# Kernel tuning notes

Measured on AMD Instinct MI355X. Metric: run time of the kernel, lower is better.

The kernel has to match this reference:

```python
import jax, jax.numpy as jnp
import numpy as np

B, N, C = 32, 256, 4096
H = 16
HEAD_DIM = C // H  # 256 == N, required by the module's math
SCALE = HEAD_DIM ** -0.5


def setup_inputs() -> dict:
    key = jax.random.key(0)
    ks = jax.random.split(key, 7)
    std = C ** -0.5
    return {
        "x1": jax.random.normal(ks[0], (B, N, C), dtype=jnp.float32),
        "x2": jax.random.normal(ks[1], (B, N, C), dtype=jnp.float32),
        "Wq": jax.random.normal(ks[2], (C, C), dtype=jnp.float32) * std,
        "Wk": jax.random.normal(ks[3], (C, C), dtype=jnp.float32) * std,
        "Wv": jax.random.normal(ks[4], (C, C), dtype=jnp.float32) * std,
        "Wp": jax.random.normal(ks[5], (C, C), dtype=jnp.float32) * std,
        "bp": jnp.zeros((C,), dtype=jnp.float32),
    }


def reference(x1, x2, Wq, Wk, Wv, Wp, bp):
    b, n, c = x1.shape
    h, hd = H, HEAD_DIM
    # QKV projections (qkv_bias=False); q pre-scaled as in source
    q = (x1 @ Wq.T) * SCALE
    k = x2 @ Wk.T
    v = x2 @ Wv.T
    split = lambda t: t.reshape(b, n, h, hd).transpose(0, 2, 1, 3)  # b h n hd
    q, k, v = split(q), split(k), split(v)
    # channel-wise attention: q^T @ k over the token axis -> [b, h, hd, hd]
    attn = jax.nn.softmax(jnp.einsum("bhni,bhnj->bhij", q, k), axis=-1)
    # attn @ v: inner dim of attn (hd) contracts with token axis of v (n == hd)
    out = jnp.einsum("bhin,bhnc->bhic", attn, v)  # [b, h, hd, hd]
    out = out.transpose(0, 2, 1, 3).reshape(b, n, c)
    x = out @ Wp.T + bp
    return (x, attn)
```

## Files before the change

### kernel.cpp

```cpp
#include <hip/hip_runtime.h>

typedef __attribute__((ext_vector_type(4))) float f32x4;
typedef __attribute__((ext_vector_type(8))) short short8;
typedef __attribute__((ext_vector_type(4))) unsigned short ushort4v;

__device__ __forceinline__ unsigned short rne_bf16(float f) {
  unsigned int u = __builtin_bit_cast(unsigned int, f);
  u += 0x7FFFu + ((u >> 16) & 1u);
  return (unsigned short)(u >> 16);
}

__device__ __forceinline__ void async16(void* lds, const void* g) {
  __builtin_amdgcn_global_load_lds(
      (const __attribute__((address_space(1))) void*)g,
      (__attribute__((address_space(3))) void*)lds, 16, 0, 0);
}

__device__ __forceinline__ f32x4 mfma16(short8 a, short8 b, f32x4 c) {
  return __builtin_amdgcn_mfma_f32_16x16x32_bf16(a, b, c, 0, 0, 0);
}

__global__ __launch_bounds__(256) void cast_k(const float* __restrict__ in,
                                              unsigned short* __restrict__ out,
                                              int n4) {
  int stride = gridDim.x * 256;
  for (int i = blockIdx.x * 256 + threadIdx.x; i < n4; i += stride) {
    float4 v = ((const float4*)in)[i];
    ushort4v o = {rne_bf16(v.x), rne_bf16(v.y), rne_bf16(v.z), rne_bf16(v.w)};
    ((ushort4v*)out)[i] = o;
  }
}

template <int MODE>
__global__ __launch_bounds__(512, 2) void gemm256(const unsigned short* __restrict__ A,
                                                  const unsigned short* __restrict__ B,
                                                  float* __restrict__ outF,
                                                  unsigned short* __restrict__ outB,
                                                  const float* __restrict__ bias,
                                                  int K, int lda, int ldb,
                                                  float scale, int gx) {
  __shared__ unsigned short lds[65536];
  const int tid = threadIdx.x;
  const int lane = tid & 63;
  const int wid = tid >> 6;
  const int wm = wid >> 2;
  const int wn = wid & 3;
  int lin = blockIdx.x;
  lin = (lin & 7) * (gridDim.x >> 3) + (lin >> 3);
  const int bx = lin % gx;
  const int by = lin / gx;
  const int m0 = by * 256, n0 = bx * 256;
  const int NT = K >> 6;

  const int gsw8 = (((tid & 3) ^ ((tid >> 3) & 3))) * 8;
  const unsigned short* gA = A + (size_t)(m0 + (tid >> 2)) * lda + gsw8;
  const unsigned short* gB = B + (size_t)(n0 + (tid >> 2)) * ldb + gsw8;
  const size_t astep = (size_t)128 * lda;
  const size_t bstep = (size_t)128 * ldb;
  unsigned short* ld0 = &lds[tid * 8];

#define STG(Q) do { \
    const int kt_ = ((Q) >> 1) * 64 + ((Q) & 1) * 32; \
    const int off_ = (((Q) >> 1) & 1) * 32768 + ((Q) & 1) * 8192; \
    const unsigned short* sA_ = gA + kt_; \
    unsigned short* dA_ = ld0 + off_; \
    async16(dA_, sA_); async16(dA_ + 4096, sA_ + astep); \
    const unsigned short* sB_ = gB + kt_; \
    unsigned short* dB_ = ld0 + 16384 + off_; \
    async16(dB_, sB_); async16(dB_ + 4096, sB_ + bstep); } while (0)

  const int rl = lane & 15;
  const int ch = (lane >> 4) ^ ((rl >> 1) & 3);
  const int aidx = wm * 4096 + rl * 32 + ch * 8;
  const int bidx = 16384 + wn * 2048 + rl * 32 + ch * 8;

  short8 af[8], bf0[4], bf1[4];
#define READ_A(base) do { \
    _Pragma("unroll") \
    for (int r_ = 0; r_ < 8; ++r_) af[r_] = *(const short8*)&lds[(base) + aidx + r_ * 512]; \
  } while (0)
#define READ_B(base, dst) do { \
    _Pragma("unroll") \
    for (int s_ = 0; s_ < 4; ++s_) dst[s_] = *(const short8*)&lds[(base) + bidx + s_ * 512]; \
  } while (0)

  f32x4 acc[8][4];
#pragma unroll
  for (int r = 0; r < 8; ++r)
#pragma unroll
    for (int s = 0; s < 4; ++s) acc[r][s] = (f32x4){0.f, 0.f, 0.f, 0.f};

#define MFMA32(bfX) do { \
    __builtin_amdgcn_s_setprio(1); \
    _Pragma("unroll") \
    for (int r_ = 0; r_ < 8; ++r_) \
      _Pragma("unroll") \
      for (int s_ = 0; s_ < 4; ++s_) acc[r_][s_] = mfma16(af[r_], bfX[s_], acc[r_][s_]); \
    __builtin_amdgcn_s_setprio(0); \
  } while (0)

  STG(0); STG(1); STG(2);
  asm volatile("s_waitcnt vmcnt(4)" ::: "memory");
  __builtin_amdgcn_s_barrier();
  READ_B(0, bf0);

  for (int t = 0; t < NT; ++t) {
    const int bb = (t & 1) * 32768;
    READ_A(bb);
    READ_B(bb + 8192, bf1);
    if (t + 1 < NT) STG(2 * t + 3);
    __builtin_amdgcn_sched_barrier(0);
    MFMA32(bf0);
    if (t + 1 < NT) asm volatile("s_waitcnt vmcnt(4)" ::: "memory");
    else            asm volatile("s_waitcnt vmcnt(0)" ::: "memory");
    __builtin_amdgcn_s_barrier();
    READ_A(bb + 8192);
    if (t + 1 < NT) {
      READ_B(((t + 1) & 1) * 32768, bf0);
      if (t + 2 < NT) STG(2 * t + 4);
    }
    __builtin_amdgcn_sched_barrier(0);
    MFMA32(bf1);
    if (t + 1 < NT) {
      if (t + 2 < NT) asm volatile("s_waitcnt vmcnt(4)" ::: "memory");
      else            asm volatile("s_waitcnt vmcnt(0)" ::: "memory");
      __builtin_amdgcn_s_barrier();
    }
  }
#undef STG
#undef READ_A
#undef READ_B
#undef MFMA32

  const int fcol = lane & 15;
  const int frow = (lane >> 4) * 4;
#pragma unroll
  for (int r = 0; r < 8; ++r) {
#pragma unroll
    for (int s = 0; s < 4; ++s) {
      f32x4 v = acc[r][s];
      const int m = m0 + wm * 128 + r * 16 + frow;
      const int n = n0 + wn * 64 + s * 16 + fcol;
      if (MODE == 0) {
        ushort4v p;
#pragma unroll
        for (int j = 0; j < 4; ++j) p[j] = rne_bf16(v[j] * scale);
        size_t d = ((size_t)((m >> 8) * 16 + (n >> 8))) * 65536 +
                   (size_t)(n & 255) * 256 + (m & 255);
        *(ushort4v*)&outB[d] = p;
      } else {
        float bv = bias[n];
#pragma unroll
        for (int j = 0; j < 4; ++j) outF[(size_t)(m + j) * 4096 + n] = v[j] + bv;
      }
    }
  }
}

template <int MODE>
__global__ __launch_bounds__(256) void gemm_bt(const unsigned short* __restrict__ Ab,
                                               const unsigned short* __restrict__ Bb,
                                               float* __restrict__ outF,
                                               unsigned short* __restrict__ outB,
                                               int K, int lda, int ldb) {
  __shared__ short Ash[128 * 32];
  __shared__ short Bsh[128 * 32];

  const int tid = threadIdx.x;
  const int lane = tid & 63;
  const int wid = tid >> 6;
  const int z = blockIdx.z;
  const int m0 = blockIdx.y * 128;
  const int n0 = blockIdx.x * 128;

  const unsigned short* A = Ab + (size_t)z * 65536;
  const unsigned short* B = Bb + (size_t)z * 65536;

  const int wm = (wid >> 1) * 64;
  const int wn = (wid & 1) * 64;
  const int fcol = lane & 15;
  const int kslot = (lane >> 4) * 8;

  f32x4 acc[4][4];
#pragma unroll
  for (int r = 0; r < 4; ++r)
#pragma unroll
    for (int s = 0; s < 4; ++s) acc[r][s] = (f32x4){0.f, 0.f, 0.f, 0.f};

  const int arow = tid >> 2;
  const int acol = (tid & 3) * 8;
  const unsigned short* gA = A + (size_t)(m0 + arow) * lda + acol;
  const unsigned short* gB = B + (size_t)(n0 + arow) * ldb + acol;
  short* lA = &Ash[tid * 8];
  short* lB = &Bsh[tid * 8];

  for (int kt = 0; kt < K; kt += 32) {
    __syncthreads();
    async16(lA, gA + kt);
    async16(lA + 2048, gA + (size_t)64 * lda + kt);
    async16(lB, gB + kt);
    async16(lB + 2048, gB + (size_t)64 * ldb + kt);
    __syncthreads();

    short8 a[4], b[4];
#pragma unroll
    for (int r = 0; r < 4; ++r)
      a[r] = *(const short8*)&Ash[(wm + r * 16 + fcol) * 32 + kslot];
#pragma unroll
    for (int s = 0; s < 4; ++s)
      b[s] = *(const short8*)&Bsh[(wn + s * 16 + fcol) * 32 + kslot];
#pragma unroll
    for (int r = 0; r < 4; ++r)
#pragma unroll
      for (int s = 0; s < 4; ++s)
        acc[r][s] = __builtin_amdgcn_mfma_f32_16x16x32_bf16(a[r], b[s], acc[r][s], 0, 0, 0);
  }

  const int frow = (lane >> 4) * 4;
#pragma unroll
  for (int r = 0; r < 4; ++r) {
#pragma unroll
    for (int s = 0; s < 4; ++s) {
      f32x4 v = acc[r][s];
      const int m = m0 + wm + r * 16 + frow;
      const int n = n0 + wn + s * 16 + fcol;
      if (MODE == 1) {
        float* C = outF + (size_t)z * 65536;
#pragma unroll
        for (int j = 0; j < 4; ++j) C[(size_t)(m + j) * 256 + n] = v[j];
      } else {
        size_t base = ((size_t)((z >> 4) * 256 + m)) * 4096 + (z & 15) * 256 + n;
#pragma unroll
        for (int j = 0; j < 4; ++j) outB[base + (size_t)j * 4096] = rne_bf16(v[j]);
      }
    }
  }
}

__global__ __launch_bounds__(256) void softmax_k(float* __restrict__ S,
                                                 unsigned short* __restrict__ P) {
  const int lane = threadIdx.x & 63;
  const size_t row = (size_t)blockIdx.x * 4 + (threadIdx.x >> 6);
  float4 x = *(const float4*)&S[row * 256 + lane * 4];
  float mx = fmaxf(fmaxf(x.x, x.y), fmaxf(x.z, x.w));
#pragma unroll
  for (int off = 32; off; off >>= 1) mx = fmaxf(mx, __shfl_xor(mx, off, 64));
  float e0 = __expf(x.x - mx), e1 = __expf(x.y - mx);
  float e2 = __expf(x.z - mx), e3 = __expf(x.w - mx);
  float s = e0 + e1 + e2 + e3;
#pragma unroll
  for (int off = 32; off; off >>= 1) s += __shfl_xor(s, off, 64);
  const float inv = 1.0f / s;
  e0 *= inv; e1 *= inv; e2 *= inv; e3 *= inv;
  *(float4*)&S[row * 256 + lane * 4] = make_float4(e0, e1, e2, e3);
  ushort4v ob = {rne_bf16(e0), rne_bf16(e1), rne_bf16(e2), rne_bf16(e3)};
  *(ushort4v*)&P[row * 256 + lane * 4] = ob;
}

extern "C" void kernel_launch(void* const* d_in, const int* in_sizes, int n_in,
                              void* d_out, int out_size, void* d_ws, size_t ws_size,
                              hipStream_t stream) {
  const float* x1 = (const float*)d_in[0];
  const float* x2 = (const float*)d_in[1];
  const float* Wq = (const float*)d_in[2];
  const float* Wk = (const float*)d_in[3];
  const float* Wv = (const float*)d_in[4];
  const float* Wp = (const float*)d_in[5];
  const float* bp = (const float*)d_in[6];

  float* outX = (float*)d_out;
  float* outA = outX + (size_t)33554432;

  unsigned short* Qt  = (unsigned short*)d_ws;
  unsigned short* Kt  = Qt + 33554432;
  unsigned short* Vt  = Kt + 33554432;
  unsigned short* x1b = Vt + 33554432;
  unsigned short* x2b = x1b + 33554432;
  unsigned short* Wb  = x2b + 33554432;

  const float SCALE = 0.0625f;

  cast_k<<<2048, 256, 0, stream>>>(x1, x1b, 8388608);
  cast_k<<<2048, 256, 0, stream>>>(x2, x2b, 8388608);

  cast_k<<<2048, 256, 0, stream>>>(Wq, Wb, 4194304);
  gemm256<0><<<512, 512, 0, stream>>>(x1b, Wb, nullptr, Qt, nullptr,
                                      4096, 4096, 4096, SCALE, 16);
  cast_k<<<2048, 256, 0, stream>>>(Wk, Wb, 4194304);
  gemm256<0><<<512, 512, 0, stream>>>(x2b, Wb, nullptr, Kt, nullptr,
                                      4096, 4096, 4096, 1.0f, 16);
  cast_k<<<2048, 256, 0, stream>>>(Wv, Wb, 4194304);
  gemm256<0><<<512, 512, 0, stream>>>(x2b, Wb, nullptr, Vt, nullptr,
                                      4096, 4096, 4096, 1.0f, 16);

  gemm_bt<1><<<dim3(2, 2, 512), 256, 0, stream>>>(Qt, Kt, outA, nullptr, 256, 256, 256);
  softmax_k<<<32768, 256, 0, stream>>>(outA, x1b);
  gemm_bt<2><<<dim3(2, 2, 512), 256, 0, stream>>>(x1b, Vt, nullptr, x2b, 256, 256, 256);

  cast_k<<<2048, 256, 0, stream>>>(Wp, Wb, 4194304);
  gemm256<3><<<512, 512, 0, stream>>>(x2b, Wb, outX, nullptr, bp,
                                      4096, 4096, 4096, 1.0f, 16);
}
```

Measured before the change: 1.323 ms.

## Split GEMM main loop into finer phases with barrier-interleaved LDS reads and staging

Restructures the bf16 MFMA GEMM main loop into per-half-tile phases. Each phase reads half of the A fragments plus B, issues the A stage, runs 16 MFMAs, then reads the other A half and issues the B stage before the next 16 MFMAs. Extra block barriers and lgkmcnt waits are added in a ping-pong style schedule. The aim is to interleave LDS reads, global-to-LDS copies and MFMAs across waves while cutting fragment registers (one B buffer instead of two). The cost is more barriers per K step and exposed LDS read latency, since B is no longer prefetched.

```diff
diff --git a/kernel.cpp b/kernel.cpp
--- a/kernel.cpp
+++ b/kernel.cpp
@@ -59,14 +59,17 @@
   const size_t bstep = (size_t)128 * ldb;
   unsigned short* ld0 = &lds[tid * 8];
 
-#define STG(Q) do { \
+#define STG_A(Q) do { \
     const int kt_ = ((Q) >> 1) * 64 + ((Q) & 1) * 32; \
     const int off_ = (((Q) >> 1) & 1) * 32768 + ((Q) & 1) * 8192; \
     const unsigned short* sA_ = gA + kt_; \
     unsigned short* dA_ = ld0 + off_; \
-    async16(dA_, sA_); async16(dA_ + 4096, sA_ + astep); \
+    async16(dA_, sA_); async16(dA_ + 4096, sA_ + astep); } while (0)
+#define STG_B(Q) do { \
+    const int kt_ = ((Q) >> 1) * 64 + ((Q) & 1) * 32; \
+    const int off_ = 16384 + (((Q) >> 1) & 1) * 32768 + ((Q) & 1) * 8192; \
     const unsigned short* sB_ = gB + kt_; \
-    unsigned short* dB_ = ld0 + 16384 + off_; \
+    unsigned short* dB_ = ld0 + off_; \
     async16(dB_, sB_); async16(dB_ + 4096, sB_ + bstep); } while (0)
 
   const int rl = lane & 15;
@@ -74,14 +77,15 @@
   const int aidx = wm * 4096 + rl * 32 + ch * 8;
   const int bidx = 16384 + wn * 2048 + rl * 32 + ch * 8;
 
-  short8 af[8], bf0[4], bf1[4];
-#define READ_A(base) do { \
+  short8 af[8], bf[4];
+#define READ_A4(base, o) do { \
     _Pragma("unroll") \
-    for (int r_ = 0; r_ < 8; ++r_) af[r_] = *(const short8*)&lds[(base) + aidx + r_ * 512]; \
+    for (int r_ = 0; r_ < 4; ++r_) \
+      af[(o) + r_] = *(const short8*)&lds[(base) + aidx + ((o) + r_) * 512]; \
   } while (0)
-#define READ_B(base, dst) do { \
+#define READ_B4(base) do { \
     _Pragma("unroll") \
-    for (int s_ = 0; s_ < 4; ++s_) dst[s_] = *(const short8*)&lds[(base) + bidx + s_ * 512]; \
+    for (int s_ = 0; s_ < 4; ++s_) bf[s_] = *(const short8*)&lds[(base) + bidx + s_ * 512]; \
   } while (0)
 
   f32x4 acc[8][4];
@@ -90,47 +94,56 @@
 #pragma unroll
     for (int s = 0; s < 4; ++s) acc[r][s] = (f32x4){0.f, 0.f, 0.f, 0.f};
 
-#define MFMA32(bfX) do { \
+#define MFMA16(o) do { \
+    _Pragma("unroll") \
+    for (int r_ = 0; r_ < 4; ++r_) \
+      _Pragma("unroll") \
+      for (int s_ = 0; s_ < 4; ++s_) \
+        acc[(o) + r_][s_] = mfma16(af[(o) + r_], bf[s_], acc[(o) + r_][s_]); \
+  } while (0)
+
+#define PHASE(P_, rb_, doStage_) do { \
+    READ_A4((rb_), 0); \
+    READ_B4((rb_)); \
+    if (doStage_) STG_A((P_) + 3); \
+    __builtin_amdgcn_sched_barrier(0); \
+    __builtin_amdgcn_s_barrier(); \
+    asm volatile("s_waitcnt lgkmcnt(0)" ::: "memory"); \
+    __builtin_amdgcn_sched_barrier(0); \
     __builtin_amdgcn_s_setprio(1); \
-    _Pragma("unroll") \
-    for (int r_ = 0; r_ < 8; ++r_) \
-      _Pragma("unroll") \
-      for (int s_ = 0; s_ < 4; ++s_) acc[r_][s_] = mfma16(af[r_], bfX[s_], acc[r_][s_]); \
+    MFMA16(0); \
     __builtin_amdgcn_s_setprio(0); \
+    __builtin_amdgcn_s_barrier(); \
+    READ_A4((rb_), 4); \
+    if (doStage_) STG_B((P_) + 3); \
+    __builtin_amdgcn_sched_barrier(0); \
+    __builtin_amdgcn_s_barrier(); \
+    asm volatile("s_waitcnt lgkmcnt(0)" ::: "memory"); \
+    __builtin_amdgcn_sched_barrier(0); \
+    __builtin_amdgcn_s_setprio(1); \
+    MFMA16(4); \
+    __builtin_amdgcn_s_setprio(0); \
+    if (doStage_) asm volatile("s_waitcnt vmcnt(4)" ::: "memory"); \
+    else          asm volatile("s_waitcnt vmcnt(0)" ::: "memory"); \
+    __builtin_amdgcn_s_barrier(); \
   } while (0)
 
-  STG(0); STG(1); STG(2);
+  STG_A(0); STG_B(0); STG_A(1); STG_B(1); STG_A(2); STG_B(2);
   asm volatile("s_waitcnt vmcnt(4)" ::: "memory");
   __builtin_amdgcn_s_barrier();
-  READ_B(0, bf0);
-
+
+  const int PMAX = 2 * NT - 1;
   for (int t = 0; t < NT; ++t) {
     const int bb = (t & 1) * 32768;
-    READ_A(bb);
-    READ_B(bb + 8192, bf1);
-    if (t + 1 < NT) STG(2 * t + 3);
-    __builtin_amdgcn_sched_barrier(0);
-    MFMA32(bf0);
-    if (t + 1 < NT) asm volatile("s_waitcnt vmcnt(4)" ::: "memory");
-    else            asm volatile("s_waitcnt vmcnt(0)" ::: "memory");
-    __builtin_amdgcn_s_barrier();
-    READ_A(bb + 8192);
-    if (t + 1 < NT) {
-      READ_B(((t + 1) & 1) * 32768, bf0);
-      if (t + 2 < NT) STG(2 * t + 4);
-    }
-    __builtin_amdgcn_sched_barrier(0);
-    MFMA32(bf1);
-    if (t + 1 < NT) {
-      if (t + 2 < NT) asm volatile("s_waitcnt vmcnt(4)" ::: "memory");
-      else            asm volatile("s_waitcnt vmcnt(0)" ::: "memory");
-      __builtin_amdgcn_s_barrier();
-    }
-  }
-#undef STG
-#undef READ_A
-#undef READ_B
-#undef MFMA32
+    PHASE(2 * t,     bb,        (2 * t + 3) <= PMAX);
+    PHASE(2 * t + 1, bb + 8192, (2 * t + 4) <= PMAX);
+  }
+#undef STG_A
+#undef STG_B
+#undef READ_A4
+#undef READ_B4
+#undef MFMA16
+#undef PHASE
 
   const int fcol = lane & 15;
   const int frow = (lane >> 4) * 4;
```

Result: slower. 1.349 ms (+2.0%).

## Fuse QK^T, softmax and PV into a single attention kernel

Applied to the files above, without the earlier changes.

Replaces the separate score GEMM, softmax kernel and attn@V GEMM with one kernel per (head, 64-row block). Scores stay in registers and the softmax uses cross-wave reductions through LDS. Normalized probabilities go to the fp32 output and to padded bf16 LDS, which feed the PV MFMA loop directly, with V double-buffered. This removes the fp32 score round trip and the bf16 P round trip through global memory and two launches. In exchange, K is reloaded per row block and LDS use is large (~69KB), which limits occupancy.

```diff
diff --git a/kernel.cpp b/kernel.cpp
--- a/kernel.cpp
+++ b/kernel.cpp
@@ -157,104 +157,174 @@
   }
 }
 
-template <int MODE>
-__global__ __launch_bounds__(256) void gemm_bt(const unsigned short* __restrict__ Ab,
-                                               const unsigned short* __restrict__ Bb,
-                                               float* __restrict__ outF,
-                                               unsigned short* __restrict__ outB,
-                                               int K, int lda, int ldb) {
-  __shared__ short Ash[128 * 32];
-  __shared__ short Bsh[128 * 32];
-
+__global__ __launch_bounds__(256) void attn_fused(const unsigned short* __restrict__ Qt,
+                                                  const unsigned short* __restrict__ Kt,
+                                                  const unsigned short* __restrict__ Vt,
+                                                  float* __restrict__ outA,
+                                                  unsigned short* __restrict__ outXb) {
+  __shared__ unsigned short sh[34560];
   const int tid = threadIdx.x;
   const int lane = tid & 63;
   const int wid = tid >> 6;
-  const int z = blockIdx.z;
-  const int m0 = blockIdx.y * 128;
-  const int n0 = blockIdx.x * 128;
-
-  const unsigned short* A = Ab + (size_t)z * 65536;
-  const unsigned short* B = Bb + (size_t)z * 65536;
-
-  const int wm = (wid >> 1) * 64;
-  const int wn = (wid & 1) * 64;
+  const int z = blockIdx.y;
+  const int m0 = blockIdx.x * 64;
+  const int wm = wid >> 1;
+  const int wn = wid & 1;
   const int fcol = lane & 15;
   const int kslot = (lane >> 4) * 8;
-
-  f32x4 acc[4][4];
-#pragma unroll
-  for (int r = 0; r < 4; ++r)
-#pragma unroll
-    for (int s = 0; s < 4; ++s) acc[r][s] = (f32x4){0.f, 0.f, 0.f, 0.f};
-
-  const int arow = tid >> 2;
-  const int acol = (tid & 3) * 8;
-  const unsigned short* gA = A + (size_t)(m0 + arow) * lda + acol;
-  const unsigned short* gB = B + (size_t)(n0 + arow) * ldb + acol;
-  short* lA = &Ash[tid * 8];
-  short* lB = &Bsh[tid * 8];
-
-  for (int kt = 0; kt < K; kt += 32) {
-    __syncthreads();
-    async16(lA, gA + kt);
-    async16(lA + 2048, gA + (size_t)64 * lda + kt);
-    async16(lB, gB + kt);
-    async16(lB + 2048, gB + (size_t)64 * ldb + kt);
-    __syncthreads();
-
-    short8 a[4], b[4];
-#pragma unroll
-    for (int r = 0; r < 4; ++r)
-      a[r] = *(const short8*)&Ash[(wm + r * 16 + fcol) * 32 + kslot];
-#pragma unroll
-    for (int s = 0; s < 4; ++s)
-      b[s] = *(const short8*)&Bsh[(wn + s * 16 + fcol) * 32 + kslot];
-#pragma unroll
-    for (int r = 0; r < 4; ++r)
-#pragma unroll
-      for (int s = 0; s < 4; ++s)
-        acc[r][s] = __builtin_amdgcn_mfma_f32_16x16x32_bf16(a[r], b[s], acc[r][s], 0, 0, 0);
-  }
-
   const int frow = (lane >> 4) * 4;
-#pragma unroll
-  for (int r = 0; r < 4; ++r) {
-#pragma unroll
-    for (int s = 0; s < 4; ++s) {
-      f32x4 v = acc[r][s];
-      const int m = m0 + wm + r * 16 + frow;
-      const int n = n0 + wn + s * 16 + fcol;
-      if (MODE == 1) {
-        float* C = outF + (size_t)z * 65536;
-#pragma unroll
-        for (int j = 0; j < 4; ++j) C[(size_t)(m + j) * 256 + n] = v[j];
-      } else {
-        size_t base = ((size_t)((z >> 4) * 256 + m)) * 4096 + (z & 15) * 256 + n;
-#pragma unroll
-        for (int j = 0; j < 4; ++j) outB[base + (size_t)j * 4096] = rne_bf16(v[j]);
+
+  const unsigned short* Qh = Qt + (size_t)z * 65536;
+  const unsigned short* Kh = Kt + (size_t)z * 65536;
+  const unsigned short* Vh = Vt + (size_t)z * 65536;
+  float* redM = (float*)&sh[33536];
+  float* redS = redM + 128;
+
+  f32x4 acc[2][8];
+#pragma unroll
+  for (int r = 0; r < 2; ++r)
+#pragma unroll
+    for (int s = 0; s < 8; ++s) acc[r][s] = (f32x4){0.f, 0.f, 0.f, 0.f};
+
+  {
+    const int arow = tid >> 2;
+    const int acol = (tid & 3) * 8;
+    const unsigned short* gQ = Qh + (size_t)(m0 + arow) * 256 + acol;
+    const unsigned short* gK = Kh + (size_t)arow * 256 + acol;
+    unsigned short* lA = &sh[tid * 8];
+    unsigned short* lB = &sh[2048 + tid * 8];
+
+    for (int kt = 0; kt < 256; kt += 32) {
+      __syncthreads();
+      async16(lA, gQ + kt);
+      async16(lB, gK + kt);
+      async16(lB + 2048, gK + (size_t)64 * 256 + kt);
+      async16(lB + 4096, gK + (size_t)128 * 256 + kt);
+      async16(lB + 6144, gK + (size_t)192 * 256 + kt);
+      __syncthreads();
+
+      short8 a[2], b[8];
+#pragma unroll
+      for (int r = 0; r < 2; ++r)
+        a[r] = *(const short8*)&sh[(wm * 32 + r * 16 + fcol) * 32 + kslot];
+#pragma unroll
+      for (int s = 0; s < 8; ++s)
+        b[s] = *(const short8*)&sh[2048 + (wn * 128 + s * 16 + fcol) * 32 + kslot];
+#pragma unroll
+      for (int r = 0; r < 2; ++r)
+#pragma unroll
+        for (int s = 0; s < 8; ++s)
+          acc[r][s] = mfma16(a[r], b[s], acc[r][s]);
+    }
+  }
+  __syncthreads();
+
+#pragma unroll
+  for (int r = 0; r < 2; ++r) {
+#pragma unroll
+    for (int j = 0; j < 4; ++j) {
+      float m = acc[r][0][j];
+#pragma unroll
+      for (int s = 1; s < 8; ++s) m = fmaxf(m, acc[r][s][j]);
+#pragma unroll
+      for (int off = 1; off < 16; off <<= 1) m = fmaxf(m, __shfl_xor(m, off, 64));
+      if (fcol == 0) redM[(wm * 32 + r * 16 + frow + j) * 2 + wn] = m;
+    }
+  }
+  __syncthreads();
+#pragma unroll
+  for (int r = 0; r < 2; ++r) {
+#pragma unroll
+    for (int j = 0; j < 4; ++j) {
+      const int rl = wm * 32 + r * 16 + frow + j;
+      const float m = fmaxf(redM[rl * 2 + 0], redM[rl * 2 + 1]);
+      float sum = 0.f;
+#pragma unroll
+      for (int s = 0; s < 8; ++s) {
+        float e = __expf(acc[r][s][j] - m);
+        acc[r][s][j] = e;
+        sum += e;
       }
-    }
-  }
-}
-
-__global__ __launch_bounds__(256) void softmax_k(float* __restrict__ S,
-                                                 unsigned short* __restrict__ P) {
-  const int lane = threadIdx.x & 63;
-  const size_t row = (size_t)blockIdx.x * 4 + (threadIdx.x >> 6);
-  float4 x = *(const float4*)&S[row * 256 + lane * 4];
-  float mx = fmaxf(fmaxf(x.x, x.y), fmaxf(x.z, x.w));
-#pragma unroll
-  for (int off = 32; off; off >>= 1) mx = fmaxf(mx, __shfl_xor(mx, off, 64));
-  float e0 = __expf(x.x - mx), e1 = __expf(x.y - mx);
-  float e2 = __expf(x.z - mx), e3 = __expf(x.w - mx);
-  float s = e0 + e1 + e2 + e3;
-#pragma unroll
-  for (int off = 32; off; off >>= 1) s += __shfl_xor(s, off, 64);
-  const float inv = 1.0f / s;
-  e0 *= inv; e1 *= inv; e2 *= inv; e3 *= inv;
-  *(float4*)&S[row * 256 + lane * 4] = make_float4(e0, e1, e2, e3);
-  ushort4v ob = {rne_bf16(e0), rne_bf16(e1), rne_bf16(e2), rne_bf16(e3)};
-  *(ushort4v*)&P[row * 256 + lane * 4] = ob;
+#pragma unroll
+      for (int off = 1; off < 16; off <<= 1) sum += __shfl_xor(sum, off, 64);
+      if (fcol == 0) redS[rl * 2 + wn] = sum;
+    }
+  }
+  __syncthreads();
+#pragma unroll
+  for (int r = 0; r < 2; ++r) {
+#pragma unroll
+    for (int j = 0; j < 4; ++j) {
+      const int rl = wm * 32 + r * 16 + frow + j;
+      const float inv = 1.0f / (redS[rl * 2 + 0] + redS[rl * 2 + 1]);
+      const size_t rowo = (size_t)z * 65536 + (size_t)(m0 + rl) * 256;
+#pragma unroll
+      for (int s = 0; s < 8; ++s) {
+        const int col = wn * 128 + s * 16 + fcol;
+        const float p = acc[r][s][j] * inv;
+        outA[rowo + col] = p;
+        sh[16384 + rl * 268 + col] = rne_bf16(p);
+      }
+    }
+  }
+  __syncthreads();
+
+  const unsigned short* gV = Vh + (size_t)(tid >> 2) * 256 + (tid & 3) * 8;
+#define STGV(kt, vb) do { \
+    _Pragma("unroll") \
+    for (int k_ = 0; k_ < 4; ++k_) \
+      async16(&sh[(vb) + tid * 8 + k_ * 2048], \
+              gV + (size_t)k_ * 64 * 256 + (kt) * 32); } while (0)
+
+  STGV(0, 0); STGV(1, 8192);
+  asm volatile("s_waitcnt vmcnt(4)" ::: "memory");
+  __builtin_amdgcn_s_barrier();
+
+  f32x4 acc2[2][8];
+#pragma unroll
+  for (int r = 0; r < 2; ++r)
+#pragma unroll
+    for (int s = 0; s < 8; ++s) acc2[r][s] = (f32x4){0.f, 0.f, 0.f, 0.f};
+
+  for (int kt = 0; kt < 8; ++kt) {
+    const int vb = (kt & 1) * 8192;
+    short8 a2[2], b2[8];
+#pragma unroll
+    for (int r = 0; r < 2; ++r)
+      a2[r] = *(const short8*)&sh[16384 + (wm * 32 + r * 16 + fcol) * 268 + kt * 32 + kslot];
+#pragma unroll
+    for (int s = 0; s < 8; ++s)
+      b2[s] = *(const short8*)&sh[vb + (wn * 128 + s * 16 + fcol) * 32 + kslot];
+#pragma unroll
+    for (int r = 0; r < 2; ++r)
+#pragma unroll
+      for (int s = 0; s < 8; ++s)
+        acc2[r][s] = mfma16(a2[r], b2[s], acc2[r][s]);
+    __builtin_amdgcn_s_barrier();
+    if (kt + 2 < 8) {
+      STGV(kt + 2, vb);
+      asm volatile("s_waitcnt vmcnt(4)" ::: "memory");
+    } else {
+      asm volatile("s_waitcnt vmcnt(0)" ::: "memory");
+    }
+    __builtin_amdgcn_s_barrier();
+  }
+#undef STGV
+
+#pragma unroll
+  for (int r = 0; r < 2; ++r) {
+#pragma unroll
+    for (int s = 0; s < 8; ++s) {
+      f32x4 v = acc2[r][s];
+      const int i0 = m0 + wm * 32 + r * 16 + frow;
+      const int c = wn * 128 + s * 16 + fcol;
+#pragma unroll
+      for (int j = 0; j < 4; ++j) {
+        size_t d = ((size_t)((z >> 4) * 256 + i0 + j)) * 4096 + (z & 15) * 256 + c;
+        outXb[d] = rne_bf16(v[j]);
+      }
+    }
+  }
 }
 
 extern "C" void kernel_launch(void* const* d_in, const int* in_sizes, int n_in,
@@ -293,9 +363,7 @@
   gemm256<0><<<512, 512, 0, stream>>>(x2b, Wb, nullptr, Vt, nullptr,
                                       4096, 4096, 4096, 1.0f, 16);
 
-  gemm_bt<1><<<dim3(2, 2, 512), 256, 0, stream>>>(Qt, Kt, outA, nullptr, 256, 256, 256);
-  softmax_k<<<32768, 256, 0, stream>>>(outA, x1b);
-  gemm_bt<2><<<dim3(2, 2, 512), 256, 0, stream>>>(x1b, Vt, nullptr, x2b, 256, 256, 256);
+  attn_fused<<<dim3(4, 512), 256, 0, stream>>>(Qt, Kt, Vt, outA, x2b);
 
   cast_k<<<2048, 256, 0, stream>>>(Wp, Wb, 4194304);
   gemm256<3><<<512, 512, 0, stream>>>(x2b, Wb, outX, nullptr, bp,
```

Result: faster. 1.264 ms (-4.4%).
